# Optimization experiments

Measured on AMD Instinct MI355X. Metric: run time of the kernel, lower is better.

## Reference

```python
import jax, jax.numpy as jnp
import numpy as np

B, S, D, H = 4, 2048, 1024, 16
HD = D // H  # head dim = 64


def setup_inputs() -> dict:
    key = jax.random.key(0)
    ks = jax.random.split(key, 8)
    s = 1.0 / np.sqrt(D)
    return {
        "query": jax.random.normal(ks[0], (B, S, D), jnp.float32),
        "key": jax.random.normal(ks[1], (B, S, D), jnp.float32),
        "value": jax.random.normal(ks[2], (B, S, D), jnp.float32),
        "wq": jax.random.normal(ks[3], (D, D), jnp.float32) * s,
        "wk": jax.random.normal(ks[4], (D, D), jnp.float32) * s,
        "wv": jax.random.normal(ks[5], (D, D), jnp.float32) * s,
        "wo": jax.random.normal(ks[6], (D, D), jnp.float32) * s,
        "bo": jax.random.normal(ks[7], (D,), jnp.float32) * s,
    }


def reference(query, key, value, wq, wk, wv, wo, bo):
    # project and split heads: [B,S,D] -> [B,H,S,HD]
    def split_heads(x, w):
        return (x @ w.T).reshape(B, S, H, HD).transpose(0, 2, 1, 3)

    q = split_heads(query, wq)
    k = split_heads(key, wk)
    v = split_heads(value, wv)
    scores = jnp.einsum('bhqd,bhkd->bhqk', q, k) / jnp.sqrt(jnp.float32(HD))
    attn = jax.nn.softmax(scores, axis=-1)
    out = jnp.einsum('bhqk,bhkd->bhqd', attn, v)
    out = out.transpose(0, 2, 1, 3).reshape(B, S, D)
    return out @ wo.T + bo
```

## Files before the change

### kernel.cpp

```cpp
#include <hip/hip_runtime.h>
#include <stdint.h>


#define NSEQ 2048
#define NDIM 1024
#define NE   8388608

typedef unsigned short u16;
typedef unsigned int   u32;
typedef __bf16 bf16x8 __attribute__((ext_vector_type(8)));
typedef float  f32x4  __attribute__((ext_vector_type(4)));

__device__ __forceinline__ u16 f2bf(float f) {
  return (u16)((__builtin_bit_cast(u32, f) + 0x8000u) >> 16);
}
__device__ __forceinline__ u32 pack_bf2(float lo, float hi) {
  u32 a = __builtin_bit_cast(u32, lo) + 0x8000u;
  u32 b = __builtin_bit_cast(u32, hi) + 0x8000u;
  return __builtin_amdgcn_perm(b, a, 0x07060302);
}

__device__ __forceinline__ void async_load16(const u16* gsrc, u16* ldst) {
  __builtin_amdgcn_global_load_lds(
      (const __attribute__((address_space(1))) void*)gsrc,
      (__attribute__((address_space(3))) void*)ldst, 16, 0, 0);
}

__device__ __forceinline__ void conv_body(const float* __restrict__ src,
                                          u16* __restrict__ dst, int blk) {
  const int i = blk * 256 + (int)threadIdx.x;
  const float4 a = ((const float4*)src)[2 * i];
  const float4 b = ((const float4*)src)[2 * i + 1];
  uint4 o;
  o.x = pack_bf2(a.x, a.y); o.y = pack_bf2(a.z, a.w);
  o.z = pack_bf2(b.x, b.y); o.w = pack_bf2(b.z, b.w);
  ((uint4*)dst)[i] = o;
}
__global__ __launch_bounds__(256) void conv_big_kernel(
    const float* __restrict__ query, const float* __restrict__ keyi,
    const float* __restrict__ value, u16* __restrict__ Xq,
    u16* __restrict__ Xk, u16* __restrict__ Xv) {
  int blk = blockIdx.x;
  const float* src; u16* dst;
  if (blk < 4096)      { src = query; dst = Xq; }
  else if (blk < 8192) { src = keyi;  dst = Xk; blk -= 4096; }
  else                 { src = value; dst = Xv; blk -= 8192; }
  conv_body(src, dst, blk);
}
__global__ __launch_bounds__(256) void conv_w_kernel(
    const float* __restrict__ wq, const float* __restrict__ wk,
    const float* __restrict__ wv, const float* __restrict__ wo,
    u16* __restrict__ Wall) {
  int blk = blockIdx.x;
  const int z = blk >> 9;
  blk &= 511;
  const float* src = (z == 0) ? wq : (z == 1) ? wk : (z == 2) ? wv : wo;
  conv_body(src, Wall + (size_t)z * 1048576, blk);
}

template <bool OUTF32, bool BIAS>
__device__ __forceinline__ void gemm_core(const u16* __restrict__ A,
                                          const u16* __restrict__ B,
                                          void* __restrict__ Yv,
                                          const float* __restrict__ bias,
                                          float scale, long m0, long n0,
                                          long ldy) {
  __shared__ u16 At[128 * 32];
  __shared__ u16 Bt[128 * 32];
  const int t    = threadIdx.x;
  const int lane = t & 63;
  const int w    = t >> 6;
  const int m    = lane & 15;
  const int q    = lane >> 4;
  const int wr   = w >> 1;
  const int wc   = w & 1;
  const int srow = t >> 2;
  const int scol = (t & 3) * 8;

  f32x4 acc[4][4];
#pragma unroll
  for (int i = 0; i < 4; i++)
#pragma unroll
    for (int j = 0; j < 4; j++) acc[i][j] = (f32x4){0.f, 0.f, 0.f, 0.f};

  for (int k0 = 0; k0 < NDIM; k0 += 32) {
    __syncthreads();
    async_load16(A + (m0 + srow) * NDIM + k0 + scol, At + w * 512);
    async_load16(A + (m0 + 64 + srow) * NDIM + k0 + scol, At + 2048 + w * 512);
    async_load16(B + (n0 + srow) * NDIM + k0 + scol, Bt + w * 512);
    async_load16(B + (n0 + 64 + srow) * NDIM + k0 + scol, Bt + 2048 + w * 512);
    __syncthreads();

    bf16x8 a[4], b[4];
#pragma unroll
    for (int mi = 0; mi < 4; mi++)
      a[mi] = *(const bf16x8*)(At + (wr * 64 + mi * 16 + m) * 32 + q * 8);
#pragma unroll
    for (int ni = 0; ni < 4; ni++)
      b[ni] = *(const bf16x8*)(Bt + (wc * 64 + ni * 16 + m) * 32 + q * 8);
#pragma unroll
    for (int mi = 0; mi < 4; mi++)
#pragma unroll
      for (int ni = 0; ni < 4; ni++)
        acc[mi][ni] = __builtin_amdgcn_mfma_f32_16x16x32_bf16(a[mi], b[ni], acc[mi][ni], 0, 0, 0);
  }

#pragma unroll
  for (int mi = 0; mi < 4; mi++) {
#pragma unroll
    for (int ni = 0; ni < 4; ni++) {
      const long row0 = m0 + wr * 64 + mi * 16 + q * 4;
      const long col  = n0 + wc * 64 + ni * 16 + m;
      float badd = 0.f;
      if (BIAS) badd = bias[col];
#pragma unroll
      for (int r = 0; r < 4; r++) {
        const float v = acc[mi][ni][r] * scale + badd;
        if (OUTF32) ((float*)Yv)[(row0 + r) * ldy + col] = v;
        else        ((u16*)Yv)[(row0 + r) * ldy + col] = f2bf(v);
      }
    }
  }
}

__global__ __launch_bounds__(256) void gemm_qkv_kernel(
    const u16* __restrict__ Xq, const u16* __restrict__ Xk,
    const u16* __restrict__ Xv, const u16* __restrict__ Wall,
    u16* __restrict__ Qp, u16* __restrict__ Kp, u16* __restrict__ Vt) {
  const int z = blockIdx.z;
  if (z < 2) {
    const u16* A = z ? Xk : Xq;
    const u16* B = Wall + (size_t)z * 1048576;
    u16* Y       = z ? Kp : Qp;
    gemm_core<false, false>(A, B, Y, nullptr, z ? 1.0f : 0.18033688f,
                            (long)blockIdx.x * 128, (long)blockIdx.y * 128, NDIM);
  } else {
    const int flat = blockIdx.y * 64 + blockIdx.x;
    const long b   = flat >> 7;
    const int rem  = flat & 127;
    gemm_core<false, false>(Wall + 2 * 1048576, Xv + b * NSEQ * NDIM,
                            Vt + b * (long)NDIM * NSEQ, nullptr, 1.0f,
                            (long)(rem >> 4) * 128, (long)(rem & 15) * 128, NSEQ);
  }
}

__global__ __launch_bounds__(256) void gemm_out_kernel(
    const u16* __restrict__ A, const u16* __restrict__ Wall,
    float* __restrict__ Y, const float* __restrict__ bias) {
  gemm_core<true, true>(A, Wall + 3 * 1048576, Y, bias, 1.0f,
                        (long)blockIdx.x * 128, (long)blockIdx.y * 128, NDIM);
}

__global__ __launch_bounds__(256, 4) void attn_kernel(
    const u16* __restrict__ Qp, const u16* __restrict__ Kp,
    const u16* __restrict__ Vtg, u16* __restrict__ Op) {
  __shared__ u16 Kt[64 * 72];
  __shared__ u16 Vt[64 * 72];
  const int t    = threadIdx.x;
  const int lane = t & 63;
  const int w    = t >> 6;
  const int m    = lane & 15;
  const int q    = lane >> 4;
  const int bh   = blockIdx.y;
  const int b    = bh >> 4;
  const int h    = bh & 15;
  const int wq0  = blockIdx.x * 128 + w * 32;
  const long base_bh = (long)b * NSEQ * NDIM + h * 64;
  const long vbase   = (long)b * NDIM * NSEQ + (long)(h * 64) * NSEQ;

  bf16x8 qf[2][2];
#pragma unroll
  for (int qi = 0; qi < 2; qi++)
#pragma unroll
    for (int ks = 0; ks < 2; ks++)
      qf[qi][ks] = *(const bf16x8*)(Qp + base_bh + (long)(wq0 + qi * 16 + m) * NDIM + ks * 32 + q * 8);

  f32x4 ot[2][4];
#pragma unroll
  for (int qi = 0; qi < 2; qi++)
#pragma unroll
    for (int mb = 0; mb < 4; mb++) ot[qi][mb] = (f32x4){0.f, 0.f, 0.f, 0.f};
  float lp[2] = {0.f, 0.f};

  const int srow = t >> 3;
  const int c8   = t & 7;
  const int scol = c8 * 8;

  const int vnb   = c8 >> 1;
  const int vbase_c = 32 * (vnb >> 1) + 4 * (vnb & 1);
  const int vcol0 = vbase_c + 8 * ((2 * c8) & 3);
  const int vcol1 = vbase_c + 8 * ((2 * c8 + 1) & 3);

  const u16* kgp = Kp + base_bh + (long)srow * NDIM + scol;
  const u16* vgp = Vtg + vbase + (long)srow * NSEQ + scol;

  int4 kr0 = *(const int4*)(kgp);
  int4 kr1 = *(const int4*)(kgp + 32l * NDIM);
  int4 vr0 = *(const int4*)(vgp);
  int4 vr1 = *(const int4*)(vgp + 32l * NSEQ);

  const f32x4 zz = (f32x4){0.f, 0.f, 0.f, 0.f};

  for (int kt = 0; kt < NSEQ / 64; kt++) {
    __syncthreads();
    *(int4*)(Kt + srow * 72 + scol)        = kr0;
    *(int4*)(Kt + (srow + 32) * 72 + scol) = kr1;
    *(uint2*)(Vt + srow * 72 + vcol0)        = make_uint2((u32)vr0.x, (u32)vr0.y);
    *(uint2*)(Vt + srow * 72 + vcol1)        = make_uint2((u32)vr0.z, (u32)vr0.w);
    *(uint2*)(Vt + (srow + 32) * 72 + vcol0) = make_uint2((u32)vr1.x, (u32)vr1.y);
    *(uint2*)(Vt + (srow + 32) * 72 + vcol1) = make_uint2((u32)vr1.z, (u32)vr1.w);
    __syncthreads();

    if (kt < NSEQ / 64 - 1) {
      const long k1 = (long)(kt + 1) * 64;
      kr0 = *(const int4*)(kgp + k1 * NDIM);
      kr1 = *(const int4*)(kgp + (k1 + 32) * NDIM);
      vr0 = *(const int4*)(vgp + k1);
      vr1 = *(const int4*)(vgp + 32l * NSEQ + k1);
    }

    f32x4 st[2][4];
    __builtin_amdgcn_s_setprio(1);
#pragma unroll
    for (int nb = 0; nb < 4; nb++) {
      bf16x8 kf = *(const bf16x8*)(Kt + (nb * 16 + m) * 72 + q * 8);
      st[0][nb] = __builtin_amdgcn_mfma_f32_16x16x32_bf16(kf, qf[0][0], zz, 0, 0, 0);
      st[1][nb] = __builtin_amdgcn_mfma_f32_16x16x32_bf16(kf, qf[1][0], zz, 0, 0, 0);
    }
#pragma unroll
    for (int nb = 0; nb < 4; nb++) {
      bf16x8 kf = *(const bf16x8*)(Kt + (nb * 16 + m) * 72 + 32 + q * 8);
      st[0][nb] = __builtin_amdgcn_mfma_f32_16x16x32_bf16(kf, qf[0][1], st[0][nb], 0, 0, 0);
      st[1][nb] = __builtin_amdgcn_mfma_f32_16x16x32_bf16(kf, qf[1][1], st[1][nb], 0, 0, 0);
    }
    __builtin_amdgcn_s_setprio(0);

    u32 pkx[2][4], pky[2][4];
#pragma unroll
    for (int qi = 0; qi < 2; qi++)
#pragma unroll
      for (int nb = 0; nb < 4; nb++) {
        const float p0 = __builtin_amdgcn_exp2f(st[qi][nb][0]);
        const float p1 = __builtin_amdgcn_exp2f(st[qi][nb][1]);
        const float p2 = __builtin_amdgcn_exp2f(st[qi][nb][2]);
        const float p3 = __builtin_amdgcn_exp2f(st[qi][nb][3]);
        lp[qi] += (p0 + p1) + (p2 + p3);
        pkx[qi][nb] = pack_bf2(p0, p1);
        pky[qi][nb] = pack_bf2(p2, p3);
      }

    __builtin_amdgcn_s_setprio(1);
#pragma unroll
    for (int ks2 = 0; ks2 < 2; ks2++) {
      bf16x8 pf[2];
#pragma unroll
      for (int qi = 0; qi < 2; qi++) {
        uint4 pw;
        pw.x = pkx[qi][2 * ks2];
        pw.y = pky[qi][2 * ks2];
        pw.z = pkx[qi][2 * ks2 + 1];
        pw.w = pky[qi][2 * ks2 + 1];
        pf[qi] = __builtin_bit_cast(bf16x8, pw);
      }
#pragma unroll
      for (int mb = 0; mb < 4; mb++) {
        bf16x8 vf = *(const bf16x8*)(Vt + (mb * 16 + m) * 72 + ks2 * 32 + q * 8);
        ot[0][mb] = __builtin_amdgcn_mfma_f32_16x16x32_bf16(vf, pf[0], ot[0][mb], 0, 0, 0);
        ot[1][mb] = __builtin_amdgcn_mfma_f32_16x16x32_bf16(vf, pf[1], ot[1][mb], 0, 0, 0);
      }
    }
    __builtin_amdgcn_s_setprio(0);
  }

  float rinv[2];
#pragma unroll
  for (int qi = 0; qi < 2; qi++) {
    float v = lp[qi];
    v += __shfl_xor(v, 16);
    v += __shfl_xor(v, 32);
    rinv[qi] = 1.0f / v;
  }

  __syncthreads();
  u16* ept = Kt + w * 1152;
#pragma unroll
  for (int qi = 0; qi < 2; qi++) {
#pragma unroll
    for (int mb = 0; mb < 4; mb++) {
      uint2 pk;
      pk.x = pack_bf2(ot[qi][mb][0] * rinv[qi], ot[qi][mb][1] * rinv[qi]);
      pk.y = pack_bf2(ot[qi][mb][2] * rinv[qi], ot[qi][mb][3] * rinv[qi]);
      *(uint2*)(ept + m * 72 + mb * 16 + q * 4) = pk;
    }
#pragma unroll
    for (int c = 0; c < 2; c++) {
      const int u   = c * 64 + lane;
      const int qr  = u >> 3;
      const int oct = u & 7;
      const int4 val = *(const int4*)(ept + qr * 72 + oct * 8);
      const long s   = wq0 + qi * 16 + qr;
      *(int4*)(Op + base_bh + s * NDIM + oct * 8) = val;
    }
  }
}

extern "C" void kernel_launch(void* const* d_in, const int* in_sizes, int n_in,
                              void* d_out, int out_size, void* d_ws, size_t ws_size,
                              hipStream_t stream) {
  const float* query = (const float*)d_in[0];
  const float* keyi  = (const float*)d_in[1];
  const float* value = (const float*)d_in[2];
  const float* wq    = (const float*)d_in[3];
  const float* wk    = (const float*)d_in[4];
  const float* wv    = (const float*)d_in[5];
  const float* wo    = (const float*)d_in[6];
  const float* bo    = (const float*)d_in[7];

  u16* ws = (u16*)d_ws;
  u16* Qp = ws;
  u16* Kp = ws + (size_t)NE;
  u16* Vt = ws + 2 * (size_t)NE;
  u16* XqO = ws + 3 * (size_t)NE;

  u16* Xk = (u16*)d_out;
  u16* Xv = (u16*)d_out + (size_t)NE;
  u16* Wall = (u16*)d_in[0];

  dim3 blk(256, 1, 1);
  conv_big_kernel<<<dim3(12288, 1, 1), blk, 0, stream>>>(query, keyi, value, XqO, Xk, Xv);
  conv_w_kernel<<<dim3(2048, 1, 1), blk, 0, stream>>>(wq, wk, wv, wo, Wall);
  gemm_qkv_kernel<<<dim3(64, 8, 3), blk, 0, stream>>>(XqO, Xk, Xv, Wall, Qp, Kp, Vt);
  attn_kernel<<<dim3(16, 64, 1), blk, 0, stream>>>(Qp, Kp, Vt, XqO);
  gemm_out_kernel<<<dim3(64, 8, 1), blk, 0, stream>>>(XqO, Wall, (float*)d_out, bo);
}
```

Before: 337.2 us.

## Double-buffer GEMM LDS tiles, remap blocks per XCD, use hardware bf16 pack

The GEMM core now double-buffers its A/B LDS tiles so the async global-to-LDS loads for the next K slice overlap the MFMA work on the current one, with one barrier per slice instead of two. The QKV and output GEMMs remap the flat block index so that blocks landing on the same XCD share M tiles (or N tiles for the V projection), aiming for better L2 reuse. The attention kernel replaces the manual add-and-permute bf16 packing with the v_cvt_pk_bf16_f32 instruction. The double buffer doubles GEMM LDS use, which may lower occupancy, and the hardware conversion may round slightly differently from the manual packing.

New measurement: 314.3 us. 1.07x faster.

```diff
diff --git a/kernel.cpp b/kernel.cpp
--- a/kernel.cpp
+++ b/kernel.cpp
@@ -18,6 +18,11 @@
   u32 a = __builtin_bit_cast(u32, lo) + 0x8000u;
   u32 b = __builtin_bit_cast(u32, hi) + 0x8000u;
   return __builtin_amdgcn_perm(b, a, 0x07060302);
+}
+__device__ __forceinline__ u32 cvt_pk_bf16(float lo, float hi) {
+  u32 r;
+  asm("v_cvt_pk_bf16_f32 %0, %1, %2" : "=v"(r) : "v"(lo), "v"(hi));
+  return r;
 }
 
 __device__ __forceinline__ void async_load16(const u16* gsrc, u16* ldst) {
@@ -65,8 +70,8 @@
                                           const float* __restrict__ bias,
                                           float scale, long m0, long n0,
                                           long ldy) {
-  __shared__ u16 At[128 * 32];
-  __shared__ u16 Bt[128 * 32];
+  __shared__ u16 At[2][128 * 32];
+  __shared__ u16 Bt[2][128 * 32];
   const int t    = threadIdx.x;
   const int lane = t & 63;
   const int w    = t >> 6;
@@ -83,26 +88,39 @@
 #pragma unroll
     for (int j = 0; j < 4; j++) acc[i][j] = (f32x4){0.f, 0.f, 0.f, 0.f};
 
-  for (int k0 = 0; k0 < NDIM; k0 += 32) {
-    __syncthreads();
-    async_load16(A + (m0 + srow) * NDIM + k0 + scol, At + w * 512);
-    async_load16(A + (m0 + 64 + srow) * NDIM + k0 + scol, At + 2048 + w * 512);
-    async_load16(B + (n0 + srow) * NDIM + k0 + scol, Bt + w * 512);
-    async_load16(B + (n0 + 64 + srow) * NDIM + k0 + scol, Bt + 2048 + w * 512);
-    __syncthreads();
-
+  const u16* Ab = A + (m0 + srow) * NDIM + scol;
+  const u16* Bb = B + (n0 + srow) * NDIM + scol;
+
+  auto stage = [&](u16* AT, u16* BT, int k0) {
+    async_load16(Ab + k0, AT + w * 512);
+    async_load16(Ab + 64l * NDIM + k0, AT + 2048 + w * 512);
+    async_load16(Bb + k0, BT + w * 512);
+    async_load16(Bb + 64l * NDIM + k0, BT + 2048 + w * 512);
+  };
+  auto step = [&](const u16* AT, const u16* BT) {
     bf16x8 a[4], b[4];
 #pragma unroll
     for (int mi = 0; mi < 4; mi++)
-      a[mi] = *(const bf16x8*)(At + (wr * 64 + mi * 16 + m) * 32 + q * 8);
+      a[mi] = *(const bf16x8*)(AT + (wr * 64 + mi * 16 + m) * 32 + q * 8);
 #pragma unroll
     for (int ni = 0; ni < 4; ni++)
-      b[ni] = *(const bf16x8*)(Bt + (wc * 64 + ni * 16 + m) * 32 + q * 8);
+      b[ni] = *(const bf16x8*)(BT + (wc * 64 + ni * 16 + m) * 32 + q * 8);
 #pragma unroll
     for (int mi = 0; mi < 4; mi++)
 #pragma unroll
       for (int ni = 0; ni < 4; ni++)
         acc[mi][ni] = __builtin_amdgcn_mfma_f32_16x16x32_bf16(a[mi], b[ni], acc[mi][ni], 0, 0, 0);
+  };
+
+  stage(At[0], Bt[0], 0);
+  __syncthreads();
+  for (int k0 = 0; k0 < NDIM; k0 += 64) {
+    stage(At[1], Bt[1], k0 + 32);
+    step(At[0], Bt[0]);
+    __syncthreads();
+    if (k0 + 64 < NDIM) stage(At[0], Bt[0], k0 + 64);
+    step(At[1], Bt[1]);
+    __syncthreads();
   }
 
 #pragma unroll
@@ -128,27 +146,37 @@
     const u16* __restrict__ Xv, const u16* __restrict__ Wall,
     u16* __restrict__ Qp, u16* __restrict__ Kp, u16* __restrict__ Vt) {
   const int z = blockIdx.z;
+  const int flat = blockIdx.y * 64 + blockIdx.x;
   if (z < 2) {
     const u16* A = z ? Xk : Xq;
     const u16* B = Wall + (size_t)z * 1048576;
     u16* Y       = z ? Kp : Qp;
+    const int xcd = flat & 7, c = flat >> 3;
+    const long mt = xcd * 8 + (c & 7);
+    const long nt = c >> 3;
     gemm_core<false, false>(A, B, Y, nullptr, z ? 1.0f : 0.18033688f,
-                            (long)blockIdx.x * 128, (long)blockIdx.y * 128, NDIM);
+                            mt * 128, nt * 128, NDIM);
   } else {
-    const int flat = blockIdx.y * 64 + blockIdx.x;
-    const long b   = flat >> 7;
-    const int rem  = flat & 127;
+    const long b  = flat >> 7;
+    const int rem = flat & 127;
+    const int xcd = rem & 7, c = rem >> 3;
+    const long nt = xcd * 2 + (c & 1);
+    const long mt = c >> 1;
     gemm_core<false, false>(Wall + 2 * 1048576, Xv + b * NSEQ * NDIM,
                             Vt + b * (long)NDIM * NSEQ, nullptr, 1.0f,
-                            (long)(rem >> 4) * 128, (long)(rem & 15) * 128, NSEQ);
+                            mt * 128, nt * 128, NSEQ);
   }
 }
 
 __global__ __launch_bounds__(256) void gemm_out_kernel(
     const u16* __restrict__ A, const u16* __restrict__ Wall,
     float* __restrict__ Y, const float* __restrict__ bias) {
+  const int flat = blockIdx.y * 64 + blockIdx.x;
+  const int xcd = flat & 7, c = flat >> 3;
+  const long mt = xcd * 8 + (c & 7);
+  const long nt = c >> 3;
   gemm_core<true, true>(A, Wall + 3 * 1048576, Y, bias, 1.0f,
-                        (long)blockIdx.x * 128, (long)blockIdx.y * 128, NDIM);
+                        mt * 128, nt * 128, NDIM);
 }
 
 __global__ __launch_bounds__(256, 4) void attn_kernel(
@@ -245,8 +273,8 @@
         const float p2 = __builtin_amdgcn_exp2f(st[qi][nb][2]);
         const float p3 = __builtin_amdgcn_exp2f(st[qi][nb][3]);
         lp[qi] += (p0 + p1) + (p2 + p3);
-        pkx[qi][nb] = pack_bf2(p0, p1);
-        pky[qi][nb] = pack_bf2(p2, p3);
+        pkx[qi][nb] = cvt_pk_bf16(p0, p1);
+        pky[qi][nb] = cvt_pk_bf16(p2, p3);
       }
 
     __builtin_amdgcn_s_setprio(1);
@@ -288,8 +316,8 @@
 #pragma unroll
     for (int mb = 0; mb < 4; mb++) {
       uint2 pk;
-      pk.x = pack_bf2(ot[qi][mb][0] * rinv[qi], ot[qi][mb][1] * rinv[qi]);
-      pk.y = pack_bf2(ot[qi][mb][2] * rinv[qi], ot[qi][mb][3] * rinv[qi]);
+      pk.x = cvt_pk_bf16(ot[qi][mb][0] * rinv[qi], ot[qi][mb][1] * rinv[qi]);
+      pk.y = cvt_pk_bf16(ot[qi][mb][2] * rinv[qi], ot[qi][mb][3] * rinv[qi]);
       *(uint2*)(ept + m * 72 + mb * 16 + q * 4) = pk;
     }
 #pragma unroll
```
